# Performance work log

Measured on AMD Instinct MI355X. Metric: run time of the kernel, lower is better.

## Reference

```python
import jax, jax.numpy as jnp
import numpy as np

B = 262144   # batch of polygon pairs
N = 8        # vertices per polygon
TWO_PI = 2.0 * np.pi


def sort_poly(p):
    # sort vertices CCW by angle about the centroid (repo's sort_poly)
    c = jnp.mean(p, axis=-2, keepdims=True)
    v = p - c
    ang = jnp.arctan2(v[..., 1], v[..., 0])
    order = jnp.argsort(ang, axis=-1)
    return jnp.take_along_axis(p, order[..., None], axis=-2)


def shoelace(p):
    # signed area, positive for CCW polygons: [..., K, 2] -> [...]
    q = jnp.roll(p, -1, axis=-2)
    return 0.5 * jnp.sum(p[..., 0] * q[..., 1] - p[..., 1] * q[..., 0], axis=-1)


def points_inside(pts, poly):
    # pts [B,K,2], poly [B,N,2] convex CCW -> bool [B,K]
    a = poly[:, None, :, :]
    e = jnp.roll(poly, -1, axis=1)[:, None, :, :] - a
    w = pts[:, :, None, :] - a
    cr = e[..., 0] * w[..., 1] - e[..., 1] * w[..., 0]
    return jnp.all(cr >= -1e-6, axis=-1)


def edge_intersections(pa, pb):
    # all pairwise edge-edge intersection points: -> pts [B,N*N,2], ok [B,N*N]
    bsz, n, _ = pa.shape
    p1 = pa[:, :, None, :]
    d1 = jnp.roll(pa, -1, axis=1)[:, :, None, :] - p1
    q1 = pb[:, None, :, :]
    d2 = jnp.roll(pb, -1, axis=1)[:, None, :, :] - q1
    denom = d1[..., 0] * d2[..., 1] - d1[..., 1] * d2[..., 0]
    safe = jnp.where(jnp.abs(denom) < 1e-9, 1.0, denom)
    r = q1 - p1
    t = (r[..., 0] * d2[..., 1] - r[..., 1] * d2[..., 0]) / safe
    u = (r[..., 0] * d1[..., 1] - r[..., 1] * d1[..., 0]) / safe
    ok = (jnp.abs(denom) >= 1e-9) & (t >= 0.0) & (t <= 1.0) & (u >= 0.0) & (u <= 1.0)
    pts = p1 + t[..., None] * d1
    return pts.reshape(bsz, n * n, 2), ok.reshape(bsz, n * n)


def convex_intersection_area(pa, pb):
    # intersection of two convex CCW polygons: candidate vertices are
    # (a-verts inside b) + (b-verts inside a) + edge-edge intersections,
    # sorted by angle around their centroid, shoelace with masked padding.
    ia = points_inside(pa, pb)
    ib = points_inside(pb, pa)
    xpts, xok = edge_intersections(pa, pb)
    cand = jnp.concatenate([pa, pb, xpts], axis=1)          # [B, 2N+N^2, 2]
    mask = jnp.concatenate([ia, ib, xok], axis=1)
    cnt = jnp.sum(mask, axis=1)
    mf = mask[..., None].astype(cand.dtype)
    ctr = jnp.sum(cand * mf, axis=1) / jnp.maximum(cnt, 1).astype(cand.dtype)[..., None]
    v = cand - ctr[:, None, :]
    ang = jnp.where(mask, jnp.arctan2(v[..., 1], v[..., 0]), 1e9)  # invalid -> end
    order = jnp.argsort(ang, axis=1)
    cand = jnp.take_along_axis(cand, order[..., None], axis=1)
    mask = jnp.take_along_axis(mask, order, axis=1)
    cand = jnp.where(mask[..., None], cand, cand[:, 0:1, :])  # pad w/ first valid pt
    area = shoelace(cand)
    return jnp.where(cnt >= 3, jnp.maximum(area, 0.0), 0.0)


def hull_area_single(pts):
    # gift wrapping (Jarvis march) over M points, accumulating CCW shoelace sum
    m = pts.shape[0]
    start = jnp.lexsort((pts[:, 0], pts[:, 1]))[0]  # lowest y, tie-break lowest x

    def step(carry, _):
        cur, d, done, acc = carry
        cp = pts[cur]
        v = pts - cp
        dist2 = jnp.sum(v * v, axis=-1)
        ang = jnp.arctan2(d[0] * v[:, 1] - d[1] * v[:, 0],
                          d[0] * v[:, 0] + d[1] * v[:, 1])
        ang = jnp.where(dist2 < 1e-16, jnp.inf, jnp.mod(ang, TWO_PI))
        nxt = jnp.argmin(ang)
        npnt = pts[nxt]
        acc = acc + jnp.where(done, 0.0, cp[0] * npnt[1] - cp[1] * npnt[0])
        done = done | (nxt == start)
        return (nxt, npnt - cp, done, acc), None

    init = (start, jnp.array([1.0, 0.0], pts.dtype), jnp.array(False),
            jnp.zeros((), pts.dtype))
    (_, _, _, acc), _ = jax.lax.scan(step, init, None, length=m)
    return 0.5 * acc


def _make_convex(key, bsz, n):
    # random convex polygons: points on random ellipses at sorted angles
    k1, k2, k3, k4 = jax.random.split(key, 4)
    th = jnp.sort(jax.random.uniform(k1, (bsz, n)) * TWO_PI, axis=1)
    rx = 0.5 + 1.5 * jax.random.uniform(k2, (bsz, 1))
    ry = 0.5 + 1.5 * jax.random.uniform(k3, (bsz, 1))
    c = jax.random.uniform(k4, (bsz, 2)) * 2.0 - 1.0
    return c[:, None, :] + jnp.stack([rx * jnp.cos(th), ry * jnp.sin(th)], axis=-1)


def setup_inputs() -> dict:
    key = jax.random.key(0)
    ka, kb = jax.random.split(key)
    a = _make_convex(ka, B, N).astype(jnp.float32)
    b = _make_convex(kb, B, N).astype(jnp.float32)
    return {"a": a, "b": b}


def reference(a, b):
    pa = sort_poly(a)
    pb = sort_poly(b)
    area_a = shoelace(pa)
    area_b = shoelace(pb)
    inter = convex_intersection_area(pa, pb)     # [B]
    union = area_a + area_b - inter              # shapely a.union(b).area
    iou = inter / union
    all_pts = jnp.concatenate([a, b], axis=1)    # [B, 2N, 2]
    ch_area = jax.vmap(hull_area_single)(all_pts)
    ciou = iou - (ch_area - union) / ch_area
    return jnp.mean(ciou)                        # sum over batch / batch_size
```

## Files before the change

kernel.cpp:

```cpp
#include <hip/hip_runtime.h>

#define TPB 256

__global__ __launch_bounds__(TPB, 2) void ciou_main(
    const float* __restrict__ A,
    const float* __restrict__ Bq,
    double* __restrict__ partial,
    int nbatch, int tail)
{
    const int t = threadIdx.x;
    const int i0 = blockIdx.x * TPB + t;
    const bool live = !tail || (i0 < nbatch);
    const int i = live ? i0 : (nbatch - 1);

    float ax0,ax1,ax2,ax3,ax4,ax5,ax6,ax7;
    float ay0,ay1,ay2,ay3,ay4,ay5,ay6,ay7;
    float bx0,bx1,bx2,bx3,bx4,bx5,bx6,bx7;
    float by0,by1,by2,by3,by4,by5,by6,by7;
    {
        const float4* pa = (const float4*)(A + (size_t)i * 16);
        const float4* pb = (const float4*)(Bq + (size_t)i * 16);
        float4 q;
        q = pa[0]; ax0=q.x; ay0=q.y; ax1=q.z; ay1=q.w;
        q = pa[1]; ax2=q.x; ay2=q.y; ax3=q.z; ay3=q.w;
        q = pa[2]; ax4=q.x; ay4=q.y; ax5=q.z; ay5=q.w;
        q = pa[3]; ax6=q.x; ay6=q.y; ax7=q.z; ay7=q.w;
        q = pb[0]; bx0=q.x; by0=q.y; bx1=q.z; by1=q.w;
        q = pb[1]; bx2=q.x; by2=q.y; bx3=q.z; by3=q.w;
        q = pb[2]; bx4=q.x; by4=q.y; bx5=q.z; by5=q.w;
        q = pb[3]; bx6=q.x; by6=q.y; bx7=q.z; by7=q.w;
    }

    float area_a = 0.5f * ((ax0*ay1-ay0*ax1) + (ax1*ay2-ay1*ax2)
                         + (ax2*ay3-ay2*ax3) + (ax3*ay4-ay3*ax4)
                         + (ax4*ay5-ay4*ax5) + (ax5*ay6-ay5*ax6)
                         + (ax6*ay7-ay6*ax7) + (ax7*ay0-ay7*ax0));
    float area_b = 0.5f * ((bx0*by1-by0*bx1) + (bx1*by2-by1*bx2)
                         + (bx2*by3-by2*bx3) + (bx3*by4-by3*bx4)
                         + (bx4*by5-by4*bx5) + (bx5*by6-by5*bx6)
                         + (bx6*by7-by6*bx7) + (bx7*by0-by7*bx0));

    float inter2 = 0.f;

#define HP(T0,T1,QX0,QY0,QX1,QY1) { \
        float ex = (QX1)-(QX0), ey = (QY1)-(QY0); \
        float aa = ex*(Py-(QY0)) - ey*(Px-(QX0)); \
        float bb = ex*Dy - ey*Dx; \
        float tc = __fdividef(-aa, bb); \
        float h = bb * 1e38f; \
        T0 = fmaxf(T0, fminf(tc, h)); \
        T1 = fminf(T1, fmaxf(tc, h)); }

#define HPB HP(t0a,t1a,bx0,by0,bx1,by1) HP(t0b,t1b,bx1,by1,bx2,by2) \
            HP(t0a,t1a,bx2,by2,bx3,by3) HP(t0b,t1b,bx3,by3,bx4,by4) \
            HP(t0a,t1a,bx4,by4,bx5,by5) HP(t0b,t1b,bx5,by5,bx6,by6) \
            HP(t0a,t1a,bx6,by6,bx7,by7) HP(t0b,t1b,bx7,by7,bx0,by0)
#define HPA HP(t0a,t1a,ax0,ay0,ax1,ay1) HP(t0b,t1b,ax1,ay1,ax2,ay2) \
            HP(t0a,t1a,ax2,ay2,ax3,ay3) HP(t0b,t1b,ax3,ay3,ax4,ay4) \
            HP(t0a,t1a,ax4,ay4,ax5,ay5) HP(t0b,t1b,ax5,ay5,ax6,ay6) \
            HP(t0a,t1a,ax6,ay6,ax7,ay7) HP(t0b,t1b,ax7,ay7,ax0,ay0)

#define EDGE(PX,PY,QX,QY,HPS) { \
        const float Px = (PX), Py = (PY); \
        const float Dx = (QX) - Px, Dy = (QY) - Py; \
        float t0a = 0.f, t1a = 1.f, t0b = 0.f, t1b = 1.f; \
        HPS \
        float dt = fminf(t1a, t1b) - fmaxf(t0a, t0b); \
        float cpd = Px*Dy - Py*Dx; \
        inter2 += fmaxf(dt, 0.f) * cpd; }

    EDGE(ax0,ay0,ax1,ay1,HPB) EDGE(ax1,ay1,ax2,ay2,HPB)
    EDGE(ax2,ay2,ax3,ay3,HPB) EDGE(ax3,ay3,ax4,ay4,HPB)
    EDGE(ax4,ay4,ax5,ay5,HPB) EDGE(ax5,ay5,ax6,ay6,HPB)
    EDGE(ax6,ay6,ax7,ay7,HPB) EDGE(ax7,ay7,ax0,ay0,HPB)
    EDGE(bx0,by0,bx1,by1,HPA) EDGE(bx1,by1,bx2,by2,HPA)
    EDGE(bx2,by2,bx3,by3,HPA) EDGE(bx3,by3,bx4,by4,HPA)
    EDGE(bx4,by4,bx5,by5,HPA) EDGE(bx5,by5,bx6,by6,HPA)
    EDGE(bx6,by6,bx7,by7,HPA) EDGE(bx7,by7,bx0,by0,HPA)

    float inter = fmaxf(0.5f * inter2, 0.f);
    float uni = area_a + area_b - inter;
    float iou = __fdividef(inter, uni);

#define MIN2(X1,Y1,X2,Y2) { \
        bool bs = ((Y2) < (Y1)) || (((Y2) == (Y1)) && ((X2) < (X1))); \
        X1 = bs ? (X2) : (X1); Y1 = bs ? (Y2) : (Y1); }
    float m0x=ax0, m0y=ay0; MIN2(m0x,m0y, ax1,ay1)
    float m1x=ax2, m1y=ay2; MIN2(m1x,m1y, ax3,ay3)
    float m2x=ax4, m2y=ay4; MIN2(m2x,m2y, ax5,ay5)
    float m3x=ax6, m3y=ay6; MIN2(m3x,m3y, ax7,ay7)
    float m4x=bx0, m4y=by0; MIN2(m4x,m4y, bx1,by1)
    float m5x=bx2, m5y=by2; MIN2(m5x,m5y, bx3,by3)
    float m6x=bx4, m6y=by4; MIN2(m6x,m6y, bx5,by5)
    float m7x=bx6, m7y=by6; MIN2(m7x,m7y, bx7,by7)
    MIN2(m0x,m0y, m1x,m1y) MIN2(m2x,m2y, m3x,m3y)
    MIN2(m4x,m4y, m5x,m5y) MIN2(m6x,m6y, m7x,m7y)
    MIN2(m0x,m0y, m2x,m2y) MIN2(m4x,m4y, m6x,m6y)
    MIN2(m0x,m0y, m4x,m4y)
    const float stx = m0x, sty = m0y;

#define SCANC(CDX,CDY,NX,NY,PX,PY) { \
        float vx = (PX) - cxv, vy = (PY) - cyv; \
        float cr = CDX*vy - CDY*vx; \
        bool take = cr < 0.f; \
        NX = take ? (PX) : NX;  NY = take ? (PY) : NY; \
        CDX = take ? vx : CDX;  CDY = take ? vy : CDY; }
#define MERGE(CDX,CDY,NX,NY,CDX2,CDY2,NX2,NY2) { \
        float cr = CDX*(CDY2) - CDY*(CDX2); \
        bool take = cr < 0.f; \
        NX = take ? (NX2) : NX;  NY = take ? (NY2) : NY; \
        CDX = take ? (CDX2) : CDX; CDY = take ? (CDY2) : CDY; }

    float cxv = stx, cyv = sty, accH = 0.f;
    float pdx = 1.f, pdy = 0.f;
    bool done = false;
#pragma unroll 1
    for (int it = 0; it < 16; ++it) {
        float ndx = -pdx, ndy = -pdy;
        float cdx0 = ndx, cdy0 = ndy, nx0 = cxv, ny0 = cyv;
        float cdx1 = ndx, cdy1 = ndy, nx1 = cxv, ny1 = cyv;
        float cdx2 = ndx, cdy2 = ndy, nx2 = cxv, ny2 = cyv;
        float cdx3 = ndx, cdy3 = ndy, nx3 = cxv, ny3 = cyv;
        float cdx4 = ndx, cdy4 = ndy, nx4 = cxv, ny4 = cyv;
        float cdx5 = ndx, cdy5 = ndy, nx5 = cxv, ny5 = cyv;
        float cdx6 = ndx, cdy6 = ndy, nx6 = cxv, ny6 = cyv;
        float cdx7 = ndx, cdy7 = ndy, nx7 = cxv, ny7 = cyv;
        SCANC(cdx0,cdy0,nx0,ny0, ax0,ay0) SCANC(cdx0,cdy0,nx0,ny0, ax1,ay1)
        SCANC(cdx1,cdy1,nx1,ny1, ax2,ay2) SCANC(cdx1,cdy1,nx1,ny1, ax3,ay3)
        SCANC(cdx2,cdy2,nx2,ny2, ax4,ay4) SCANC(cdx2,cdy2,nx2,ny2, ax5,ay5)
        SCANC(cdx3,cdy3,nx3,ny3, ax6,ay6) SCANC(cdx3,cdy3,nx3,ny3, ax7,ay7)
        SCANC(cdx4,cdy4,nx4,ny4, bx0,by0) SCANC(cdx4,cdy4,nx4,ny4, bx1,by1)
        SCANC(cdx5,cdy5,nx5,ny5, bx2,by2) SCANC(cdx5,cdy5,nx5,ny5, bx3,by3)
        SCANC(cdx6,cdy6,nx6,ny6, bx4,by4) SCANC(cdx6,cdy6,nx6,ny6, bx5,by5)
        SCANC(cdx7,cdy7,nx7,ny7, bx6,by6) SCANC(cdx7,cdy7,nx7,ny7, bx7,by7)
        MERGE(cdx0,cdy0,nx0,ny0, cdx1,cdy1,nx1,ny1)
        MERGE(cdx2,cdy2,nx2,ny2, cdx3,cdy3,nx3,ny3)
        MERGE(cdx4,cdy4,nx4,ny4, cdx5,cdy5,nx5,ny5)
        MERGE(cdx6,cdy6,nx6,ny6, cdx7,cdy7,nx7,ny7)
        MERGE(cdx0,cdy0,nx0,ny0, cdx2,cdy2,nx2,ny2)
        MERGE(cdx4,cdy4,nx4,ny4, cdx6,cdy6,nx6,ny6)
        MERGE(cdx0,cdy0,nx0,ny0, cdx4,cdy4,nx4,ny4)
        accH += done ? 0.f : (cxv*ny0 - cyv*nx0);
        done = done || (nx0 == stx && ny0 == sty);
        pdx = cdx0; pdy = cdy0;
        cxv = nx0; cyv = ny0;
        if (__all(done)) break;
    }
    float ch = 0.5f * accH;

    float val = iou - __fdividef(ch - uni, ch);
    float v = live ? val : 0.f;

    #pragma unroll
    for (int off = 32; off > 0; off >>= 1) v += __shfl_down(v, off);
    __shared__ float wsum[4];
    int lane = t & 63, wid = t >> 6;
    if (lane == 0) wsum[wid] = v;
    __syncthreads();
    if (t == 0) {
        partial[blockIdx.x] = (double)wsum[0] + (double)wsum[1]
                            + (double)wsum[2] + (double)wsum[3];
    }
}

__global__ __launch_bounds__(256) void ciou_finalize(
    const double* __restrict__ partial, float* __restrict__ out,
    int nparts, int nbatch)
{
    double v = 0.0;
    for (int j = threadIdx.x; j < nparts; j += 256) v += partial[j];
    #pragma unroll
    for (int off = 32; off > 0; off >>= 1) v += __shfl_down(v, off);
    __shared__ double s[4];
    int lane = threadIdx.x & 63, wid = threadIdx.x >> 6;
    if (lane == 0) s[wid] = v;
    __syncthreads();
    if (threadIdx.x == 0)
        out[0] = (float)((s[0] + s[1] + s[2] + s[3]) / (double)nbatch);
}

extern "C" void kernel_launch(void* const* d_in, const int* in_sizes, int n_in,
                              void* d_out, int out_size, void* d_ws, size_t ws_size,
                              hipStream_t stream) {
    const float* a = (const float*)d_in[0];
    const float* b = (const float*)d_in[1];
    float* out = (float*)d_out;
    int nbatch = in_sizes[0] / 16;
    int nblocks = (nbatch + TPB - 1) / TPB;
    int tail = (nblocks * TPB != nbatch) ? 1 : 0;
    double* partial = (double*)d_ws;
    ciou_main<<<nblocks, TPB, 0, stream>>>(a, b, partial, nbatch, tail);
    ciou_finalize<<<1, 256, 0, stream>>>(partial, out, nblocks, nbatch);
}
```

Before: 101.4 us.

## Reuse vertex-edge cross products across clipping steps via shared orientation terms

```diff
diff --git a/kernel.cpp b/kernel.cpp
--- a/kernel.cpp
+++ b/kernel.cpp
@@ -2,7 +2,7 @@
 
 #define TPB 256
 
-__global__ __launch_bounds__(TPB, 2) void ciou_main(
+__global__ __launch_bounds__(TPB, 4) void ciou_main(
     const float* __restrict__ A,
     const float* __restrict__ Bq,
     double* __restrict__ partial,
@@ -31,52 +31,78 @@
         q = pb[3]; bx6=q.x; by6=q.y; bx7=q.z; by7=q.w;
     }
 
-    float area_a = 0.5f * ((ax0*ay1-ay0*ax1) + (ax1*ay2-ay1*ax2)
-                         + (ax2*ay3-ay2*ax3) + (ax3*ay4-ay3*ax4)
-                         + (ax4*ay5-ay4*ax5) + (ax5*ay6-ay5*ax6)
-                         + (ax6*ay7-ay6*ax7) + (ax7*ay0-ay7*ax0));
-    float area_b = 0.5f * ((bx0*by1-by0*bx1) + (bx1*by2-by1*bx2)
-                         + (bx2*by3-by2*bx3) + (bx3*by4-by3*bx4)
-                         + (bx4*by5-by4*bx5) + (bx5*by6-by5*bx6)
-                         + (bx6*by7-by6*bx7) + (bx7*by0-by7*bx0));
+#define MKCA(I,IN) float ca##I = ax##I*ay##IN - ay##I*ax##IN;
+#define MKCB(I,IN) float cb##I = bx##I*by##IN - by##I*bx##IN;
+    MKCA(0,1) MKCA(1,2) MKCA(2,3) MKCA(3,4)
+    MKCA(4,5) MKCA(5,6) MKCA(6,7) MKCA(7,0)
+    MKCB(0,1) MKCB(1,2) MKCB(2,3) MKCB(3,4)
+    MKCB(4,5) MKCB(5,6) MKCB(6,7) MKCB(7,0)
+    float area_a = 0.5f * (((ca0+ca1)+(ca2+ca3)) + ((ca4+ca5)+(ca6+ca7)));
+    float area_b = 0.5f * (((cb0+cb1)+(cb2+cb3)) + ((cb4+cb5)+(cb6+cb7)));
 
     float inter2 = 0.f;
 
-#define HP(T0,T1,QX0,QY0,QX1,QY1) { \
-        float ex = (QX1)-(QX0), ey = (QY1)-(QY0); \
-        float aa = ex*(Py-(QY0)) - ey*(Px-(QX0)); \
-        float bb = ex*Dy - ey*Dx; \
-        float tc = __fdividef(-aa, bb); \
+#define DTST(I) float t0a##I=0.f,t1a##I=1.f,t0b##I=0.f,t1b##I=1.f;
+#define PU(I,IN,T0P,T1P) { \
+        float bb = s##IN - s##I; \
+        float tc = __fdividef(-s##I, bb); \
         float h = bb * 1e38f; \
-        T0 = fmaxf(T0, fminf(tc, h)); \
-        T1 = fminf(T1, fmaxf(tc, h)); }
-
-#define HPB HP(t0a,t1a,bx0,by0,bx1,by1) HP(t0b,t1b,bx1,by1,bx2,by2) \
-            HP(t0a,t1a,bx2,by2,bx3,by3) HP(t0b,t1b,bx3,by3,bx4,by4) \
-            HP(t0a,t1a,bx4,by4,bx5,by5) HP(t0b,t1b,bx5,by5,bx6,by6) \
-            HP(t0a,t1a,bx6,by6,bx7,by7) HP(t0b,t1b,bx7,by7,bx0,by0)
-#define HPA HP(t0a,t1a,ax0,ay0,ax1,ay1) HP(t0b,t1b,ax1,ay1,ax2,ay2) \
-            HP(t0a,t1a,ax2,ay2,ax3,ay3) HP(t0b,t1b,ax3,ay3,ax4,ay4) \
-            HP(t0a,t1a,ax4,ay4,ax5,ay5) HP(t0b,t1b,ax5,ay5,ax6,ay6) \
-            HP(t0a,t1a,ax6,ay6,ax7,ay7) HP(t0b,t1b,ax7,ay7,ax0,ay0)
-
-#define EDGE(PX,PY,QX,QY,HPS) { \
-        const float Px = (PX), Py = (PY); \
-        const float Dx = (QX) - Px, Dy = (QY) - Py; \
-        float t0a = 0.f, t1a = 1.f, t0b = 0.f, t1b = 1.f; \
-        HPS \
-        float dt = fminf(t1a, t1b) - fmaxf(t0a, t0b); \
-        float cpd = Px*Dy - Py*Dx; \
-        inter2 += fmaxf(dt, 0.f) * cpd; }
-
-    EDGE(ax0,ay0,ax1,ay1,HPB) EDGE(ax1,ay1,ax2,ay2,HPB)
-    EDGE(ax2,ay2,ax3,ay3,HPB) EDGE(ax3,ay3,ax4,ay4,HPB)
-    EDGE(ax4,ay4,ax5,ay5,HPB) EDGE(ax5,ay5,ax6,ay6,HPB)
-    EDGE(ax6,ay6,ax7,ay7,HPB) EDGE(ax7,ay7,ax0,ay0,HPB)
-    EDGE(bx0,by0,bx1,by1,HPA) EDGE(bx1,by1,bx2,by2,HPA)
-    EDGE(bx2,by2,bx3,by3,HPA) EDGE(bx3,by3,bx4,by4,HPA)
-    EDGE(bx4,by4,bx5,by5,HPA) EDGE(bx5,by5,bx6,by6,HPA)
-    EDGE(bx6,by6,bx7,by7,HPA) EDGE(bx7,by7,bx0,by0,HPA)
+        T0P##I = fmaxf(T0P##I, fminf(tc, h)); \
+        T1P##I = fminf(T1P##I, fmaxf(tc, h)); }
+
+    {
+        DTST(0) DTST(1) DTST(2) DTST(3) DTST(4) DTST(5) DTST(6) DTST(7)
+#define DM1(I) float M##I = ax##I*by0 - ay##I*bx0;
+        DM1(0) DM1(1) DM1(2) DM1(3) DM1(4) DM1(5) DM1(6) DM1(7)
+#define P1N(I,BXN,BYN,CBJ) \
+        float N##I = ax##I*(BYN) - ay##I*(BXN); \
+        float s##I = (M##I - N##I) + (CBJ); M##I = N##I;
+#define P1STEP(BXN,BYN,CBJ,T0P,T1P) { \
+        P1N(0,BXN,BYN,CBJ) P1N(1,BXN,BYN,CBJ) P1N(2,BXN,BYN,CBJ) \
+        P1N(3,BXN,BYN,CBJ) P1N(4,BXN,BYN,CBJ) P1N(5,BXN,BYN,CBJ) \
+        P1N(6,BXN,BYN,CBJ) P1N(7,BXN,BYN,CBJ) \
+        PU(0,1,T0P,T1P) PU(1,2,T0P,T1P) PU(2,3,T0P,T1P) PU(3,4,T0P,T1P) \
+        PU(4,5,T0P,T1P) PU(5,6,T0P,T1P) PU(6,7,T0P,T1P) PU(7,0,T0P,T1P) }
+        P1STEP(bx1,by1,cb0,t0a,t1a)
+        P1STEP(bx2,by2,cb1,t0b,t1b)
+        P1STEP(bx3,by3,cb2,t0a,t1a)
+        P1STEP(bx4,by4,cb3,t0b,t1b)
+        P1STEP(bx5,by5,cb4,t0a,t1a)
+        P1STEP(bx6,by6,cb5,t0b,t1b)
+        P1STEP(bx7,by7,cb6,t0a,t1a)
+        P1STEP(bx0,by0,cb7,t0b,t1b)
+#define PE1(I) { \
+        float dt = fminf(t1a##I,t1b##I) - fmaxf(t0a##I,t0b##I); \
+        inter2 += fmaxf(dt, 0.f) * ca##I; }
+        PE1(0) PE1(1) PE1(2) PE1(3) PE1(4) PE1(5) PE1(6) PE1(7)
+    }
+
+    {
+        DTST(0) DTST(1) DTST(2) DTST(3) DTST(4) DTST(5) DTST(6) DTST(7)
+#define DM2(J) float M##J = ax0*by##J - ay0*bx##J;
+        DM2(0) DM2(1) DM2(2) DM2(3) DM2(4) DM2(5) DM2(6) DM2(7)
+#define P2N(J,AXN,AYN,CAI) \
+        float N##J = (AXN)*by##J - (AYN)*bx##J; \
+        float s##J = (N##J - M##J) + (CAI); M##J = N##J;
+#define P2STEP(AXN,AYN,CAI,T0P,T1P) { \
+        P2N(0,AXN,AYN,CAI) P2N(1,AXN,AYN,CAI) P2N(2,AXN,AYN,CAI) \
+        P2N(3,AXN,AYN,CAI) P2N(4,AXN,AYN,CAI) P2N(5,AXN,AYN,CAI) \
+        P2N(6,AXN,AYN,CAI) P2N(7,AXN,AYN,CAI) \
+        PU(0,1,T0P,T1P) PU(1,2,T0P,T1P) PU(2,3,T0P,T1P) PU(3,4,T0P,T1P) \
+        PU(4,5,T0P,T1P) PU(5,6,T0P,T1P) PU(6,7,T0P,T1P) PU(7,0,T0P,T1P) }
+        P2STEP(ax1,ay1,ca0,t0a,t1a)
+        P2STEP(ax2,ay2,ca1,t0b,t1b)
+        P2STEP(ax3,ay3,ca2,t0a,t1a)
+        P2STEP(ax4,ay4,ca3,t0b,t1b)
+        P2STEP(ax5,ay5,ca4,t0a,t1a)
+        P2STEP(ax6,ay6,ca5,t0b,t1b)
+        P2STEP(ax7,ay7,ca6,t0a,t1a)
+        P2STEP(ax0,ay0,ca7,t0b,t1b)
+#define PE2(J) { \
+        float dt = fminf(t1a##J,t1b##J) - fmaxf(t0a##J,t0b##J); \
+        inter2 += fmaxf(dt, 0.f) * cb##J; }
+        PE2(0) PE2(1) PE2(2) PE2(3) PE2(4) PE2(5) PE2(6) PE2(7)
+    }
 
     float inter = fmaxf(0.5f * inter2, 0.f);
     float uni = area_a + area_b - inter;
```

After: 111.7 us. 1.1x slower.
